# Kernel optimization log

Hardware: AMD Instinct MI355X
Metric: run time of the kernel (lower is better)

## Reference

```python
import jax, jax.numpy as jnp
import numpy as np

EPS = 1e-5
D, H, W = 2, 4, 4          # fixed patch grid from the rearrange string
P = 8                       # p1*p2*p3 = 2*2*2 tokens per patch


def setup_inputs() -> dict:
    key = jax.random.key(0)
    k1, k2, k3, k4, k5 = jax.random.split(key, 5)
    c, heads = 128, 8
    B = 16 * D * H * W  # 512 patches (b=16)
    emb = jax.random.normal(k1, (B, P, c), dtype=jnp.float32)
    s = 1.0 / np.sqrt(c)
    Wq = jax.random.normal(k2, (c, c * heads), dtype=jnp.float32) * s
    Wk = jax.random.normal(k3, (c, c * heads), dtype=jnp.float32) * s
    Wv = jax.random.normal(k4, (c, c * heads), dtype=jnp.float32) * s
    Wout = jax.random.normal(k5, (c * heads, c), dtype=jnp.float32) * (1.0 / np.sqrt(c * heads))
    return {"emb": emb, "Wq": Wq, "Wk": Wk, "Wv": Wv, "Wout": Wout}


def reference(emb, Wq, Wk, Wv, Wout):
    B, n, c = emb.shape            # B = b*32, n = 8
    heads = Wq.shape[1] // c
    b = B // (D * H * W)

    q = emb @ Wq                   # (B, 8, c*heads)
    k = emb @ Wk
    v = emb @ Wv

    # '(p) (c heads)' -> heads c p  /  heads p c
    mh_q = q.reshape(B, P, c, heads).transpose(0, 3, 2, 1)   # (B, heads, c, P)
    mh_k = k.reshape(B, P, c, heads).transpose(0, 3, 1, 2)   # (B, heads, P, c)
    mh_v = v.reshape(B, P, c, heads).transpose(0, 3, 2, 1)   # (B, heads, c, P)

    attn = jnp.einsum('bhcp,bhpe->bhce', mh_q, mh_k)         # (B, heads, c, c) channel scores

    # InstanceNorm2d(num_heads): normalize each (patch, head) c x c map (biased var)
    mu = attn.mean(axis=(2, 3), keepdims=True)
    var = attn.var(axis=(2, 3), keepdims=True)
    attn = (attn - mu) * jax.lax.rsqrt(var + EPS)

    attn = jax.nn.softmax(attn, axis=3)
    ctx = jnp.einsum('bhce,bhep->bhcp', attn, mh_v)          # (B, heads, c, P)

    # '(b d h w) heads c (p1 p2 p3) -> b (d p1 h p2 w p3) (c heads)'
    ctx = ctx.reshape(b, D, H, W, heads, c, 2, 2, 2)
    ctx = ctx.transpose(0, 1, 6, 2, 7, 3, 8, 5, 4)           # b d p1 h p2 w p3 c heads
    ctx = ctx.reshape(b, D * 2 * H * 2 * W * 2, c * heads)   # (b, 256, c*heads)

    return ctx @ Wout                                        # (b, 256, c)
```

## Files before the change

### kernel.cpp

```cpp
#include <hip/hip_runtime.h>
#include <hip/hip_bf16.h>
#include <math.h>


typedef short bfrag __attribute__((ext_vector_type(8)));
typedef float f32x4 __attribute__((ext_vector_type(4)));

static __device__ __forceinline__ short f2bf(float x) {
    __hip_bfloat16 h = __float2bfloat16(x);
    return __builtin_bit_cast(short, h);
}
static __device__ __forceinline__ bfrag bzero() {
    bfrag z;
    #pragma unroll
    for (int j = 0; j < 8; ++j) z[j] = 0;
    return z;
}

__global__ __launch_bounds__(256) void convertW(
    const float* __restrict__ Wq, const float* __restrict__ Wk,
    const float* __restrict__ Wv, const float* __restrict__ Wout,
    short* __restrict__ Wp, short* __restrict__ Wout_pt,
    float* __restrict__ out)
{
    __shared__ short lt[128 * 33];
    const int b = blockIdx.x, t = threadIdx.x;

    {
        float4* o4 = (float4*)out;
        const int zb = b * 1024 + t;
        #pragma unroll
        for (int k = 0; k < 4; ++k)
            o4[zb + k * 256] = make_float4(0.f, 0.f, 0.f, 0.f);
    }

    if (b < 96) {
        const int x = b >> 5, h = (b >> 2) & 7, k0 = (b & 3) * 32;
        const float* W = (x == 0) ? Wq : (x == 1) ? Wk : Wv;
        #pragma unroll 4
        for (int rr = 0; rr < 16; ++rr) {
            const int k = rr * 2 + (t >> 7);
            const int i = t & 127;
            lt[k * 129 + i] = f2bf(W[(k0 + k) * 1024 + i * 8 + h]);
        }
        __syncthreads();
        short* dst = Wp + (x * 8 + h) * 16384;
        #pragma unroll
        for (int pp = 0; pp < 4; ++pp) {
            const int i  = pp * 32 + (t >> 3);
            const int kk = (t & 7) * 4;
            short4 v;
            v.x = lt[(kk + 0) * 129 + i]; v.y = lt[(kk + 1) * 129 + i];
            v.z = lt[(kk + 2) * 129 + i]; v.w = lt[(kk + 3) * 129 + i];
            *(short4*)&dst[i * 128 + k0 + kk] = v;
        }
    } else {
        const int b2 = b - 96, h = b2 >> 2, c0 = (b2 & 3) * 32;
        #pragma unroll 4
        for (int rr = 0; rr < 16; ++rr) {
            const int i = rr * 8 + (t >> 5);
            const int c = t & 31;
            lt[i * 33 + c] = f2bf(Wout[(i * 8 + h) * 128 + c0 + c]);
        }
        __syncthreads();
        short* dst = Wout_pt + h * 16384;
        #pragma unroll
        for (int pp = 0; pp < 4; ++pp) {
            const int c  = pp * 8 + (t >> 5);
            const int i0 = (t & 31) * 4;
            short4 v;
            v.x = lt[(i0 + 0) * 33 + c]; v.y = lt[(i0 + 1) * 33 + c];
            v.z = lt[(i0 + 2) * 33 + c]; v.w = lt[(i0 + 3) * 33 + c];
            *(short4*)&dst[(c0 + c) * 128 + i0] = v;
        }
    }
}

#define QT   0
#define KT   4096
#define QN   8192
#define KN   12288
#define VS   16384
#define CTXo 16384

__global__ __launch_bounds__(256, 4) void attn4(
    const float* __restrict__ emb,
    const short* __restrict__ Wp,
    const short* __restrict__ Wout_pt,
    float* __restrict__ out)
{
    __shared__ short lds[20480];
    const int bid = blockIdx.x;
    const int pg  = bid >> 3;
    const int h   = bid & 7;
    const int t   = threadIdx.x;
    const int w    = t >> 6;
    const int lane = t & 63;
    const int m16  = lane & 15;
    const int quad = lane >> 4;
    const int q8   = quad * 8;

    {
        bfrag a[2][4];
        #pragma unroll
        for (int tm = 0; tm < 2; ++tm)
            #pragma unroll
            for (int ks = 0; ks < 4; ++ks) {
                const float* er = emb + (size_t)(pg*32 + tm*16 + m16) * 128 + ks*32 + q8;
                const float4 x0 = *(const float4*)er;
                const float4 x1 = *(const float4*)(er + 4);
                bfrag f;
                f[0]=f2bf(x0.x); f[1]=f2bf(x0.y); f[2]=f2bf(x0.z); f[3]=f2bf(x0.w);
                f[4]=f2bf(x1.x); f[5]=f2bf(x1.y); f[6]=f2bf(x1.z); f[7]=f2bf(x1.w);
                a[tm][ks] = f;
            }

        #pragma unroll
        for (int tt = 0; tt < 6; ++tt) {
            const int nt = w * 6 + tt;
            const int x  = nt >> 3;
            const int i0 = (nt & 7) * 16;
            const short* Wb = Wp + ((x*8 + h)*128 + i0 + m16) * 128;
            bfrag bb[4];
            #pragma unroll
            for (int ks = 0; ks < 4; ++ks)
                bb[ks] = *(const bfrag*)&Wb[ks*32 + q8];
            f32x4 c0 = {0.f,0.f,0.f,0.f}, c1 = {0.f,0.f,0.f,0.f};
            #pragma unroll
            for (int ks = 0; ks < 4; ++ks) {
                c0 = __builtin_amdgcn_mfma_f32_16x16x32_bf16(a[0][ks], bb[ks], c0, 0,0,0);
                c1 = __builtin_amdgcn_mfma_f32_16x16x32_bf16(a[1][ks], bb[ks], c1, 0,0,0);
            }
            #pragma unroll
            for (int tm = 0; tm < 2; ++tm) {
                const f32x4 cc = tm ? c1 : c0;
                const int mrow0 = tm*16 + quad*4;
                const int pl = mrow0 >> 3;
                const int p0 = mrow0 & 7;
                const int col = i0 + m16;
                if (x == 0) {
                    short4 v;
                    v.x = f2bf(cc[0]); v.y = f2bf(cc[1]);
                    v.z = f2bf(cc[2]); v.w = f2bf(cc[3]);
                    *(short4*)&lds[QT + pl*1024 + col*8 + p0] = v;
                    #pragma unroll
                    for (int r = 0; r < 4; ++r)
                        lds[QN + pl*1024 + (p0 + r)*128 + col] = f2bf(cc[r]);
                } else if (x == 1) {
                    short4 v;
                    v.x = f2bf(cc[0]); v.y = f2bf(cc[1]);
                    v.z = f2bf(cc[2]); v.w = f2bf(cc[3]);
                    *(short4*)&lds[KT + pl*1024 + col*8 + p0] = v;
                    #pragma unroll
                    for (int r = 0; r < 4; ++r)
                        lds[KN + pl*1024 + (p0 + r)*128 + col] = f2bf(cc[r]);
                } else {
                    const int g = (((nt & 7) ^ (((pl & 1) << 1) | (p0 >> 2))) << 4);
                    #pragma unroll
                    for (int r = 0; r < 4; ++r)
                        lds[VS + pl*1024 + (p0 + r)*128 + g + m16] = f2bf(cc[r]);
                }
            }
        }
    }
    __syncthreads();

    float rs2, nbias;
    {
        bfrag gq[4], gk[4], gs[4], ones;
        #pragma unroll
        for (int j = 0; j < 8; ++j) ones[j] = (short)0x3F80;
        #pragma unroll
        for (int ks = 0; ks < 4; ++ks) {
            gq[ks] = (m16 < 8) ? *(const bfrag*)&lds[QN + w*1024 + m16*128 + ks*32 + q8] : bzero();
            gk[ks] = (m16 < 8) ? *(const bfrag*)&lds[KN + w*1024 + m16*128 + ks*32 + q8] : bzero();
            gs[ks] = (m16 < 8) ? *(const bfrag*)&lds[QN + w*1024 + m16*128 + ks*32 + q8]
                               : *(const bfrag*)&lds[KN + w*1024 + (m16 - 8)*128 + ks*32 + q8];
        }
        f32x4 cg = {0.f,0.f,0.f,0.f}, ch = {0.f,0.f,0.f,0.f}, cs = {0.f,0.f,0.f,0.f};
        #pragma unroll
        for (int ks = 0; ks < 4; ++ks) {
            cg = __builtin_amdgcn_mfma_f32_16x16x32_bf16(gq[ks], gq[ks], cg, 0,0,0);
            ch = __builtin_amdgcn_mfma_f32_16x16x32_bf16(gk[ks], gk[ks], ch, 0,0,0);
            cs = __builtin_amdgcn_mfma_f32_16x16x32_bf16(gs[ks], ones,  cs, 0,0,0);
        }
        float gh = 0.f, sp = 0.f;
        #pragma unroll
        for (int r = 0; r < 4; ++r) {
            gh = fmaf(cg[r], ch[r], gh);
            sp = fmaf(cs[r], __shfl_xor(cs[r], 32), sp);
        }
        sp += __shfl_xor(sp, 16);
        #pragma unroll
        for (int off = 1; off <= 32; off <<= 1)
            gh += __shfl_xor(gh, off);
        const float mean = sp * (1.f / 16384.f);
        const float var  = gh * (1.f / 16384.f) - mean * mean;
        rs2   = rsqrtf(var + 1e-5f) * 1.44269504f;
        nbias = -mean * rs2;
    }

    bfrag bs[8], av[4];
    #pragma unroll
    for (int nt = 0; nt < 8; ++nt)
        bs[nt] = (quad == 0) ? *(const bfrag*)&lds[KT + w*1024 + (nt*16 + m16)*8] : bzero();
    #pragma unroll
    for (int ks = 0; ks < 4; ++ks) {
        if (m16 < 8) {
            const int g = (((2*ks + (quad >> 1)) ^ (((w & 1) << 1) | (m16 >> 2))) << 4);
            av[ks] = *(const bfrag*)&lds[VS + w*1024 + m16*128 + g + (quad & 1)*8];
        } else if (m16 == 8) {
            bfrag o;
            #pragma unroll
            for (int j = 0; j < 8; ++j) o[j] = (short)0x3F80;
            av[ks] = o;
        } else
            av[ks] = bzero();
    }
    __syncthreads();

    short* ps = &lds[QN + w*2048];
    f32x4 c[8];
    {
        const bfrag am = (quad == 0) ? *(const bfrag*)&lds[QT + w*1024 + m16*8] : bzero();
        #pragma unroll
        for (int nt = 0; nt < 8; ++nt) {
            f32x4 z = {0.f,0.f,0.f,0.f};
            c[nt] = __builtin_amdgcn_mfma_f32_16x16x32_bf16(am, bs[nt], z, 0,0,0);
        }
    }
    #pragma unroll 1
    for (int mb = 0; mb < 8; ++mb) {
        #pragma unroll
        for (int nt = 0; nt < 8; ++nt)
            #pragma unroll
            for (int r = 0; r < 4; ++r) {
                const int row = quad*4 + r;
                ps[row*128 + ((nt ^ quad) << 4) + m16] =
                    f2bf(__builtin_amdgcn_exp2f(fmaf(c[nt][r], rs2, nbias)));
            }
        if (mb < 7) {
            const bfrag am = (quad == 0)
                ? *(const bfrag*)&lds[QT + w*1024 + ((mb+1)*16 + m16)*8] : bzero();
            #pragma unroll
            for (int nt = 0; nt < 8; ++nt) {
                f32x4 z = {0.f,0.f,0.f,0.f};
                c[nt] = __builtin_amdgcn_mfma_f32_16x16x32_bf16(am, bs[nt], z, 0,0,0);
            }
        }
        f32x4 cc = {0.f,0.f,0.f,0.f};
        #pragma unroll
        for (int ks = 0; ks < 4; ++ks) {
            const bfrag bp = *(const bfrag*)
                &ps[m16*128 + (((2*ks + (quad >> 1)) ^ (m16 >> 2)) << 4) + (quad & 1)*8];
            cc = __builtin_amdgcn_mfma_f32_16x16x32_bf16(av[ks], bp, cc, 0,0,0);
        }
        const float s  = __shfl(cc[0], 32 + m16);
        const float is = 1.0f / s;
        if (quad < 2) {
            #pragma unroll
            for (int r = 0; r < 4; ++r)
                lds[CTXo + w*1024 + (quad*4 + r)*128 + mb*16 + m16] = f2bf(cc[r] * is);
        }
    }

    bfrag ac[4];
    #pragma unroll
    for (int ks = 0; ks < 4; ++ks)
        ac[ks] = (m16 < 8) ? *(const bfrag*)&lds[CTXo + w*1024 + m16*128 + ks*32 + q8]
                           : bzero();
    const short* Wo = Wout_pt + h * 16384;
    const int pat = pg*4 + w;
    const int bb = pat >> 5, rem = pat & 31;
    const int dd = rem >> 4, hh2 = (rem >> 2) & 3, ww2 = rem & 3;
    #pragma unroll 1
    for (int nt = 0; nt < 8; ++nt) {
        f32x4 cc = {0.f,0.f,0.f,0.f};
        #pragma unroll
        for (int ks = 0; ks < 4; ++ks) {
            const bfrag wb = *(const bfrag*)&Wo[(nt*16 + m16)*128 + ks*32 + q8];
            cc = __builtin_amdgcn_mfma_f32_16x16x32_bf16(ac[ks], wb, cc, 0,0,0);
        }
        if (quad < 2) {
            #pragma unroll
            for (int r = 0; r < 4; ++r) {
                const int orow = bb*256
                    + ((((dd*2 + quad)*4 + hh2)*2 + (r >> 1))*4 + ww2)*2 + (r & 1);
                atomicAdd(&out[(size_t)orow*128 + nt*16 + m16], cc[r]);
            }
        }
    }
}

extern "C" void kernel_launch(void* const* d_in, const int* in_sizes, int n_in,
                              void* d_out, int out_size, void* d_ws, size_t ws_size,
                              hipStream_t stream) {
    const float* emb  = (const float*)d_in[0];
    const float* Wq   = (const float*)d_in[1];
    const float* Wk   = (const float*)d_in[2];
    const float* Wv   = (const float*)d_in[3];
    const float* Wout = (const float*)d_in[4];
    float* out = (float*)d_out;

    short* Wp      = (short*)d_ws;
    short* Wout_pt = Wp + 393216;

    convertW<<<128, 256, 0, stream>>>(Wq, Wk, Wv, Wout, Wp, Wout_pt, out);
    attn4<<<1024, 256, 0, stream>>>(emb, Wp, Wout_pt, out);
}
```

Before: 109.6 us.

## Restructure attention loop to compute transposed scores per key band with swizzled LDS

Reorders the attention so that scores are computed per key-channel band (K as A operand, Q as B operand) and exponentials are immediately consumed by the P·V MFMA, accumulating eight output tiles in registers instead of looping over query blocks. Also XOR-swizzles the QN/KN and context LDS layouts to reduce bank conflicts on row-major stores and fragment loads. This trades more live accumulator registers for fewer serialized shuffles and stores, and it may raise register pressure at four waves per SIMD.

```diff
diff --git a/kernel.cpp b/kernel.cpp
--- a/kernel.cpp
+++ b/kernel.cpp
@@ -81,7 +81,7 @@
 #define QN   8192
 #define KN   12288
 #define VS   16384
-#define CTXo 16384
+#define CTXK 4096
 
 __global__ __launch_bounds__(256, 4) void attn4(
     const float* __restrict__ emb,
@@ -138,6 +138,7 @@
                 const int pl = mrow0 >> 3;
                 const int p0 = mrow0 & 7;
                 const int col = i0 + m16;
+                const int cb  = nt & 7;
                 if (x == 0) {
                     short4 v;
                     v.x = f2bf(cc[0]); v.y = f2bf(cc[1]);
@@ -145,7 +146,8 @@
                     *(short4*)&lds[QT + pl*1024 + col*8 + p0] = v;
                     #pragma unroll
                     for (int r = 0; r < 4; ++r)
-                        lds[QN + pl*1024 + (p0 + r)*128 + col] = f2bf(cc[r]);
+                        lds[QN + pl*1024 + (p0 + r)*128
+                            + ((cb ^ ((p0 + r) & 3)) << 4) + m16] = f2bf(cc[r]);
                 } else if (x == 1) {
                     short4 v;
                     v.x = f2bf(cc[0]); v.y = f2bf(cc[1]);
@@ -153,9 +155,10 @@
                     *(short4*)&lds[KT + pl*1024 + col*8 + p0] = v;
                     #pragma unroll
                     for (int r = 0; r < 4; ++r)
-                        lds[KN + pl*1024 + (p0 + r)*128 + col] = f2bf(cc[r]);
+                        lds[KN + pl*1024 + (p0 + r)*128
+                            + ((cb ^ ((p0 + r) & 3)) << 4) + m16] = f2bf(cc[r]);
                 } else {
-                    const int g = (((nt & 7) ^ (((pl & 1) << 1) | (p0 >> 2))) << 4);
+                    const int g = ((cb ^ (((pl & 1) << 1) | (p0 >> 2))) << 4);
                     #pragma unroll
                     for (int r = 0; r < 4; ++r)
                         lds[VS + pl*1024 + (p0 + r)*128 + g + m16] = f2bf(cc[r]);
@@ -172,10 +175,11 @@
         for (int j = 0; j < 8; ++j) ones[j] = (short)0x3F80;
         #pragma unroll
         for (int ks = 0; ks < 4; ++ks) {
-            gq[ks] = (m16 < 8) ? *(const bfrag*)&lds[QN + w*1024 + m16*128 + ks*32 + q8] : bzero();
-            gk[ks] = (m16 < 8) ? *(const bfrag*)&lds[KN + w*1024 + m16*128 + ks*32 + q8] : bzero();
-            gs[ks] = (m16 < 8) ? *(const bfrag*)&lds[QN + w*1024 + m16*128 + ks*32 + q8]
-                               : *(const bfrag*)&lds[KN + w*1024 + (m16 - 8)*128 + ks*32 + q8];
+            const int bswz = (((2*ks + (quad >> 1)) ^ (m16 & 3)) << 4) + (quad & 1)*8;
+            gq[ks] = (m16 < 8) ? *(const bfrag*)&lds[QN + w*1024 + m16*128 + bswz] : bzero();
+            gk[ks] = (m16 < 8) ? *(const bfrag*)&lds[KN + w*1024 + m16*128 + bswz] : bzero();
+            gs[ks] = (m16 < 8) ? *(const bfrag*)&lds[QN + w*1024 + m16*128 + bswz]
+                               : *(const bfrag*)&lds[KN + w*1024 + (m16 - 8)*128 + bswz];
         }
         f32x4 cg = {0.f,0.f,0.f,0.f}, ch = {0.f,0.f,0.f,0.f}, cs = {0.f,0.f,0.f,0.f};
         #pragma unroll
@@ -203,7 +207,7 @@
     bfrag bs[8], av[4];
     #pragma unroll
     for (int nt = 0; nt < 8; ++nt)
-        bs[nt] = (quad == 0) ? *(const bfrag*)&lds[KT + w*1024 + (nt*16 + m16)*8] : bzero();
+        bs[nt] = (quad == 0) ? *(const bfrag*)&lds[QT + w*1024 + (nt*16 + m16)*8] : bzero();
     #pragma unroll
     for (int ks = 0; ks < 4; ++ks) {
         if (m16 < 8) {
@@ -219,74 +223,79 @@
     }
     __syncthreads();
 
-    short* ps = &lds[QN + w*2048];
-    f32x4 c[8];
-    {
-        const bfrag am = (quad == 0) ? *(const bfrag*)&lds[QT + w*1024 + m16*8] : bzero();
-        #pragma unroll
-        for (int nt = 0; nt < 8; ++nt) {
-            f32x4 z = {0.f,0.f,0.f,0.f};
-            c[nt] = __builtin_amdgcn_mfma_f32_16x16x32_bf16(am, bs[nt], z, 0,0,0);
-        }
-    }
-    #pragma unroll 1
-    for (int mb = 0; mb < 8; ++mb) {
-        #pragma unroll
-        for (int nt = 0; nt < 8; ++nt)
-            #pragma unroll
-            for (int r = 0; r < 4; ++r) {
-                const int row = quad*4 + r;
-                ps[row*128 + ((nt ^ quad) << 4) + m16] =
-                    f2bf(__builtin_amdgcn_exp2f(fmaf(c[nt][r], rs2, nbias)));
-            }
-        if (mb < 7) {
-            const bfrag am = (quad == 0)
-                ? *(const bfrag*)&lds[QT + w*1024 + ((mb+1)*16 + m16)*8] : bzero();
+    short* ps = &lds[(w == 0) ? 0 : (4096 + (w << 12))];
+    const int key2 = m16 >> 2;
+    const int rowoff = m16 * 32;
+    f32x4 cc[8];
+    #pragma unroll
+    for (int nt = 0; nt < 8; ++nt) cc[nt] = (f32x4){0.f,0.f,0.f,0.f};
+
+    #pragma unroll
+    for (int ks = 0; ks < 4; ++ks) {
+        #pragma unroll
+        for (int bb = 0; bb < 2; ++bb) {
+            const int band = ks*2 + bb;
+            const bfrag amk = (quad == 0)
+                ? *(const bfrag*)&lds[KT + w*1024 + (band*16 + m16)*8] : bzero();
+            const int tw = (((bb*2 + (quad >> 1)) ^ key2) << 3) + (quad & 1)*4;
             #pragma unroll
             for (int nt = 0; nt < 8; ++nt) {
                 f32x4 z = {0.f,0.f,0.f,0.f};
-                c[nt] = __builtin_amdgcn_mfma_f32_16x16x32_bf16(am, bs[nt], z, 0,0,0);
-            }
-        }
-        f32x4 cc = {0.f,0.f,0.f,0.f};
-        #pragma unroll
-        for (int ks = 0; ks < 4; ++ks) {
-            const bfrag bp = *(const bfrag*)
-                &ps[m16*128 + (((2*ks + (quad >> 1)) ^ (m16 >> 2)) << 4) + (quad & 1)*8];
-            cc = __builtin_amdgcn_mfma_f32_16x16x32_bf16(av[ks], bp, cc, 0,0,0);
-        }
-        const float s  = __shfl(cc[0], 32 + m16);
+                const f32x4 s4 = __builtin_amdgcn_mfma_f32_16x16x32_bf16(amk, bs[nt], z, 0,0,0);
+                short4 v;
+                v.x = f2bf(__builtin_amdgcn_exp2f(fmaf(s4[0], rs2, nbias)));
+                v.y = f2bf(__builtin_amdgcn_exp2f(fmaf(s4[1], rs2, nbias)));
+                v.z = f2bf(__builtin_amdgcn_exp2f(fmaf(s4[2], rs2, nbias)));
+                v.w = f2bf(__builtin_amdgcn_exp2f(fmaf(s4[3], rs2, nbias)));
+                *(short4*)&ps[nt*512 + rowoff + tw] = v;
+            }
+        }
+        #pragma unroll
+        for (int nt = 0; nt < 8; ++nt) {
+            const bfrag bp = *(const bfrag*)&ps[nt*512 + rowoff + ((quad ^ key2) << 3)];
+            cc[nt] = __builtin_amdgcn_mfma_f32_16x16x32_bf16(av[ks], bp, cc[nt], 0,0,0);
+        }
+    }
+
+    #pragma unroll
+    for (int nt = 0; nt < 8; ++nt) {
+        const float s  = __shfl(cc[nt][0], 32 + m16);
         const float is = 1.0f / s;
         if (quad < 2) {
             #pragma unroll
-            for (int r = 0; r < 4; ++r)
-                lds[CTXo + w*1024 + (quad*4 + r)*128 + mb*16 + m16] = f2bf(cc[r] * is);
+            for (int r = 0; r < 4; ++r) {
+                const int p = quad*4 + r;
+                lds[CTXK + w*1024 + p*128 + ((nt ^ (p & 3)) << 4) + m16] =
+                    f2bf(cc[nt][r] * is);
+            }
         }
     }
 
     bfrag ac[4];
     #pragma unroll
     for (int ks = 0; ks < 4; ++ks)
-        ac[ks] = (m16 < 8) ? *(const bfrag*)&lds[CTXo + w*1024 + m16*128 + ks*32 + q8]
-                           : bzero();
+        ac[ks] = (m16 < 8)
+            ? *(const bfrag*)&lds[CTXK + w*1024 + m16*128
+                  + (((2*ks + (quad >> 1)) ^ (m16 & 3)) << 4) + (quad & 1)*8]
+            : bzero();
     const short* Wo = Wout_pt + h * 16384;
     const int pat = pg*4 + w;
-    const int bb = pat >> 5, rem = pat & 31;
+    const int bb2 = pat >> 5, rem = pat & 31;
     const int dd = rem >> 4, hh2 = (rem >> 2) & 3, ww2 = rem & 3;
     #pragma unroll 1
     for (int nt = 0; nt < 8; ++nt) {
-        f32x4 cc = {0.f,0.f,0.f,0.f};
+        f32x4 cc2 = {0.f,0.f,0.f,0.f};
         #pragma unroll
         for (int ks = 0; ks < 4; ++ks) {
             const bfrag wb = *(const bfrag*)&Wo[(nt*16 + m16)*128 + ks*32 + q8];
-            cc = __builtin_amdgcn_mfma_f32_16x16x32_bf16(ac[ks], wb, cc, 0,0,0);
+            cc2 = __builtin_amdgcn_mfma_f32_16x16x32_bf16(ac[ks], wb, cc2, 0,0,0);
         }
         if (quad < 2) {
             #pragma unroll
             for (int r = 0; r < 4; ++r) {
-                const int orow = bb*256
+                const int orow = bb2*256
                     + ((((dd*2 + quad)*4 + hh2)*2 + (r >> 1))*4 + ww2)*2 + (r & 1);
-                atomicAdd(&out[(size_t)orow*128 + nt*16 + m16], cc[r]);
+                atomicAdd(&out[(size_t)orow*128 + nt*16 + m16], cc2[r]);
             }
         }
     }
```

After: 104.0 us. -5.2%, faster.
